# Kernel tuning notes

Hardware: AMD Instinct MI355X
Metric: run time of the kernel (lower is better)

The kernel has to match this reference:

```python
import jax, jax.numpy as jnp
import numpy as np

B, S, D, H = 2, 2048, 1024, 16
HD = D // H  # head_dim = 64
ROPE_BASE = 10000.0


def setup_inputs() -> dict:
    key = jax.random.key(0)
    ks = jax.random.split(key, 5)
    scale = 1.0 / np.sqrt(D)
    return {
        "x": jax.random.normal(ks[0], (B, S, D), dtype=jnp.float32),
        "Wq": jax.random.normal(ks[1], (D, D), dtype=jnp.float32) * scale,
        "Wk": jax.random.normal(ks[2], (D, D), dtype=jnp.float32) * scale,
        "Wv": jax.random.normal(ks[3], (D, D), dtype=jnp.float32) * scale,
        "Wo": jax.random.normal(ks[4], (D, D), dtype=jnp.float32) * scale,
    }


def _rotate_half(x):
    x1, x2 = x[..., : HD // 2], x[..., HD // 2:]
    return jnp.concatenate((-x2, x1), axis=-1)


def _rope_cos_sin(seq_len):
    inv_freq = 1.0 / (ROPE_BASE ** (jnp.arange(0, HD, 2, dtype=jnp.float32) / HD))
    t = jnp.arange(seq_len, dtype=jnp.float32)
    freqs = jnp.outer(t, inv_freq)          # [S, HD/2]
    emb = jnp.concatenate((freqs, freqs), -1)  # [S, HD]
    return jnp.cos(emb), jnp.sin(emb)


def reference(x, Wq, Wk, Wv, Wo):
    # projections (torch Linear: y = x @ W.T), split heads -> [B, H, S, HD]
    def proj(W):
        return (x @ W.T).reshape(B, S, H, HD).transpose(0, 2, 1, 3)

    q, k, v = proj(Wq), proj(Wk), proj(Wv)

    cos, sin = _rope_cos_sin(S)  # [S, HD] each, broadcast over B, H
    q = q * cos + _rotate_half(q) * sin
    k = k * cos + _rotate_half(k) * sin

    scale = 1.0 / np.sqrt(HD)
    scores = jnp.einsum("bhsd,bhtd->bhst", q, k) * scale  # [B,H,S,S]
    attn = jax.nn.softmax(scores, axis=-1)
    out = jnp.einsum("bhst,bhtd->bhsd", attn, v)           # [B,H,S,HD]
    out = out.transpose(0, 2, 1, 3).reshape(B, S, D)
    return out @ Wo.T
```

## Files before the change

kernel.cpp:

```cpp
#include <hip/hip_runtime.h>
#include <hip/hip_bf16.h>
#include <math.h>
#include <stdint.h>

typedef __bf16 bf16;
typedef __bf16 bf16x8 __attribute__((ext_vector_type(8)));
typedef __bf16 bf16x4 __attribute__((ext_vector_type(4)));
typedef float  f32x4  __attribute__((ext_vector_type(4)));

#define MFMA16(a,b,c) __builtin_amdgcn_mfma_f32_16x16x32_bf16((a),(b),(c),0,0,0)
#define GLOAD_LDS16(g, l) \
  __builtin_amdgcn_global_load_lds((__attribute__((address_space(1))) void*)(g), \
                                   (__attribute__((address_space(3))) void*)(l), 16, 0, 0)

static constexpr int kB  = 2;
static constexpr int kS  = 2048;
static constexpr int kD  = 1024;
static constexpr int kH  = 16;
static constexpr int kHD = 64;
static constexpr int kM  = kB * kS;
static constexpr float kExpC = 0.125f * 1.44269504f;

__global__ void cvt_all(const float* __restrict__ x,
                        const float* __restrict__ wq, const float* __restrict__ wk,
                        const float* __restrict__ wv, const float* __restrict__ wo,
                        bf16* __restrict__ xb,
                        bf16* __restrict__ wqb, bf16* __restrict__ wkb,
                        bf16* __restrict__ wvb, bf16* __restrict__ wob,
                        float2* __restrict__ rtab)
{
  const int i = blockIdx.x * 256 + threadIdx.x;
  const int NX4 = (kM * kD) / 4;
  const int NW4 = (kD * kD) / 4;
  if (i >= NX4 + 4 * NW4) {
    const int idx = i - (NX4 + 4 * NW4);
    const int s = idx >> 5, d = idx & 31;
    const float f = exp2f(-(float)d * 0.4152410118609203f);
    float sn, cs;
    sincosf((float)s * f, &sn, &cs);
    rtab[idx] = make_float2(cs, sn);
    return;
  }
  const float* src; bf16* dst; int off;
  if (i < NX4) { src = x; dst = xb; off = i; }
  else {
    const int j = i - NX4;
    const int seg = j >> 18;
    off = j & (NW4 - 1);
    src = (seg == 0) ? wq : (seg == 1) ? wk : (seg == 2) ? wv : wo;
    dst = (seg == 0) ? wqb : (seg == 1) ? wkb : (seg == 2) ? wvb : wob;
  }
  const float4 v = ((const float4*)src)[off];
  bf16x4 o = { (bf16)v.x, (bf16)v.y, (bf16)v.z, (bf16)v.w };
  ((bf16x4*)dst)[off] = o;
}

__device__ __forceinline__ void gemm_core_128(
    const bf16* __restrict__ A, const bf16* __restrict__ Bw,
    int m0, int n0, int K, bf16* aT, bf16* bT, f32x4 acc[4][4])
{
  const int t = threadIdx.x, lane = t & 63, wave = t >> 6;
  const int wm = wave >> 1, wn = wave & 1;
  const int srow = lane >> 2;
  const int scol = (lane & 3) * 8;
  for (int k0 = 0; k0 < K; k0 += 32) {
    __syncthreads();
#pragma unroll
    for (int c = 0; c < 2; ++c) {
      const int row = c * 64 + wave * 16 + srow;
      const bf16* ga = A  + (size_t)(m0 + row) * K + k0 + scol;
      const bf16* gb = Bw + (size_t)(n0 + row) * K + k0 + scol;
      GLOAD_LDS16(ga, aT + c * 2048 + wave * 512);
      GLOAD_LDS16(gb, bT + c * 2048 + wave * 512);
    }
    __syncthreads();
    bf16x8 af[4], bfr[4];
#pragma unroll
    for (int i = 0; i < 4; ++i) {
      af[i]  = *(const bf16x8*)(aT + (wm * 64 + i * 16 + (lane & 15)) * 32 + (lane >> 4) * 8);
      bfr[i] = *(const bf16x8*)(bT + (wn * 64 + i * 16 + (lane & 15)) * 32 + (lane >> 4) * 8);
    }
#pragma unroll
    for (int i = 0; i < 4; ++i)
#pragma unroll
      for (int j = 0; j < 4; ++j)
        acc[i][j] = MFMA16(af[i], bfr[j], acc[i][j]);
  }
}

__global__ __launch_bounds__(256) void proj_qkv(
    const bf16* __restrict__ xb,
    const bf16* __restrict__ wqb, const bf16* __restrict__ wkb, const bf16* __restrict__ wvb,
    bf16* __restrict__ Qb, bf16* __restrict__ Kb, bf16* __restrict__ Vb,
    const float2* __restrict__ rtab)
{
  __shared__ __align__(16) bf16 aT[4096];
  __shared__ __align__(16) bf16 bT[4096];
  const int z = blockIdx.z;
  const bf16* Ww = (z == 0) ? wqb : (z == 1) ? wkb : wvb;
  bf16*       Op = (z == 0) ? Qb  : (z == 1) ? Kb  : Vb;
  const int m0 = blockIdx.x * 128, n0 = blockIdx.y * 128;
  f32x4 acc[4][4] = {};
  gemm_core_128(xb, Ww, m0, n0, kD, aT, bT, acc);

  const int lane = threadIdx.x & 63, wave = threadIdx.x >> 6;
  const int wm = wave >> 1, wn = wave & 1, quad = lane >> 4, lc = lane & 15;
  const int hh = (n0 >> 6) + wn;
  if (z == 2) {
#pragma unroll
    for (int i = 0; i < 4; ++i)
#pragma unroll
      for (int r = 0; r < 4; ++r) {
        const int m = m0 + wm * 64 + i * 16 + quad * 4 + r;
        const int bidx = m >> 11, s = m & 2047;
        bf16* dst = Op + ((size_t)(bidx * kH + hh) * kS + s) * kHD;
#pragma unroll
        for (int j = 0; j < 4; ++j) dst[j * 16 + lc] = (bf16)acc[i][j][r];
      }
  } else {
    const float f = (z == 0) ? kExpC : 1.0f;
#pragma unroll
    for (int j = 0; j < 2; ++j) {
      const int d = j * 16 + lc;
#pragma unroll
      for (int i = 0; i < 4; ++i)
#pragma unroll
        for (int r = 0; r < 4; ++r) {
          const int m = m0 + wm * 64 + i * 16 + quad * 4 + r;
          const int bidx = m >> 11, s = m & 2047;
          const float2 cs = rtab[s * 32 + d];
          const float v0 = acc[i][j][r], v1 = acc[i][j + 2][r];
          bf16* dst = Op + ((size_t)(bidx * kH + hh) * kS + s) * kHD;
          dst[d]      = (bf16)((v0 * cs.x - v1 * cs.y) * f);
          dst[d + 32] = (bf16)((v1 * cs.x + v0 * cs.y) * f);
        }
    }
  }
}

__global__ __launch_bounds__(256) void transpose_v(
    const bf16* __restrict__ Vb, bf16* __restrict__ Vt)
{
  __shared__ __align__(16) bf16 buf[128 * 72];
  const int t = threadIdx.x;
  const int kc = blockIdx.x, bh = blockIdx.y;
  const bf16* src = Vb + ((size_t)bh * kS + kc * 128) * kHD;
  {
    const int srow = t >> 1, half = (t & 1) * 32;
#pragma unroll
    for (int u = 0; u < 4; ++u)
      *(uint4*)&buf[srow * 72 + half + u * 8] = *(const uint4*)(src + srow * kHD + half + u * 8);
  }
  __syncthreads();
  {
    const int d = t & 63, c = t >> 6;
    bf16 tmp[32];
#pragma unroll
    for (int e = 0; e < 32; ++e) tmp[e] = buf[(c * 32 + e) * 72 + d];
    bf16* dst = Vt + ((size_t)bh * kHD + d) * kS + kc * 128 + c * 32;
#pragma unroll
    for (int u = 0; u < 4; ++u)
      *(uint4*)(dst + u * 8) = *(const uint4*)&tmp[u * 8];
  }
}

__global__ __launch_bounds__(256, 2) void attn(
    const bf16* __restrict__ Qb, const bf16* __restrict__ Kb,
    const bf16* __restrict__ Vt, bf16* __restrict__ Ob)
{
  __shared__ __align__(16) bf16 kT[128 * 72];
  __shared__ __align__(16) bf16 vT[64 * 136];
  const int t = threadIdx.x, lane = t & 63, wave = t >> 6;
  const int quad = lane >> 4, lc = lane & 15;
  const int qt = blockIdx.x, bh = blockIdx.y;
  const size_t base = (size_t)bh * kS * kHD;
  const bf16* Qp = Qb + base + (size_t)qt * 128 * kHD;
  const bf16* Kp = Kb + base;
  const bf16* Vp = Vt + base;

  bf16x8 qf[2][2];
#pragma unroll
  for (int tm = 0; tm < 2; ++tm)
#pragma unroll
    for (int ks = 0; ks < 2; ++ks)
      qf[tm][ks] = *(const bf16x8*)(Qp + (wave * 32 + tm * 16 + lc) * kHD + ks * 32 + quad * 8);

  f32x4 oacc[2][4] = {};
  f32x4 lacc[2] = {};
  const bf16 one = (bf16)1.0f;
  const bf16x8 ones = { one, one, one, one, one, one, one, one };

  const int srow = t >> 1, shalf = (t & 1) * 32;
  const int vd = t >> 2, vc = t & 3;

  for (int kt = 0; kt < kS / 128; ++kt) {
    __syncthreads();
    {
      const bf16* ksrc = Kp + (size_t)(kt * 128 + srow) * kHD + shalf;
#pragma unroll
      for (int u = 0; u < 4; ++u)
        *(uint4*)&kT[srow * 72 + shalf + u * 8] = *(const uint4*)(ksrc + u * 8);
      const bf16* vsrc = Vp + (size_t)vd * kS + kt * 128 + vc * 32;
#pragma unroll
      for (int u = 0; u < 4; ++u)
        *(uint4*)&vT[vd * 136 + vc * 32 + u * 8] = *(const uint4*)(vsrc + u * 8);
    }
    __syncthreads();

    bf16x8 kf[8][2];
#pragma unroll
    for (int nk = 0; nk < 8; ++nk)
#pragma unroll
      for (int ks = 0; ks < 2; ++ks)
        kf[nk][ks] = *(const bf16x8*)&kT[(nk * 16 + lc) * 72 + ks * 32 + quad * 8];

    bf16x8 pfrag[2][4];
#pragma unroll
    for (int tm = 0; tm < 2; ++tm) {
      f32x4 sc[8] = {};
#pragma unroll
      for (int nk = 0; nk < 8; ++nk) {
        sc[nk] = MFMA16(kf[nk][0], qf[tm][0], sc[nk]);
        sc[nk] = MFMA16(kf[nk][1], qf[tm][1], sc[nk]);
      }
#pragma unroll
      for (int kp = 0; kp < 4; ++kp) {
        bf16x8 p;
#pragma unroll
        for (int j = 0; j < 4; ++j) {
          p[j]     = (bf16)__builtin_amdgcn_exp2f(sc[2 * kp][j]);
          p[j + 4] = (bf16)__builtin_amdgcn_exp2f(sc[2 * kp + 1][j]);
        }
        pfrag[tm][kp] = p;
      }
    }

#pragma unroll
    for (int kp = 0; kp < 4; ++kp)
#pragma unroll
      for (int tm = 0; tm < 2; ++tm)
        lacc[tm] = MFMA16(pfrag[tm][kp], ones, lacc[tm]);

#pragma unroll
    for (int nd = 0; nd < 4; ++nd)
#pragma unroll
      for (int kp = 0; kp < 4; ++kp) {
        const bf16x4 lo = *(const bf16x4*)&vT[(nd * 16 + lc) * 136 + kp * 32 + quad * 4];
        const bf16x4 hi = *(const bf16x4*)&vT[(nd * 16 + lc) * 136 + kp * 32 + 16 + quad * 4];
        const bf16x8 vfr = __builtin_shufflevector(lo, hi, 0, 1, 2, 3, 4, 5, 6, 7);
#pragma unroll
        for (int tm = 0; tm < 2; ++tm)
          oacc[tm][nd] = MFMA16(pfrag[tm][kp], vfr, oacc[tm][nd]);
      }
  }

  const int b = bh >> 4, h = bh & 15;
#pragma unroll
  for (int tm = 0; tm < 2; ++tm)
#pragma unroll
    for (int r = 0; r < 4; ++r) {
      const float inv = 1.0f / lacc[tm][r];
      const int s = qt * 128 + wave * 32 + tm * 16 + quad * 4 + r;
      bf16* dst = Ob + ((size_t)(b * kS + s)) * kD + h * kHD;
#pragma unroll
      for (int nd = 0; nd < 4; ++nd)
        dst[nd * 16 + lc] = (bf16)(oacc[tm][nd][r] * inv);
    }
}

__global__ __launch_bounds__(256) void out_proj(
    const bf16* __restrict__ Ab, const bf16* __restrict__ wob, float* __restrict__ Cout)
{
  __shared__ __align__(16) bf16 aT[4096];
  __shared__ __align__(16) bf16 bT[4096];
  const int m0 = blockIdx.x * 128, n0 = blockIdx.y * 128;
  f32x4 acc[4][4] = {};
  gemm_core_128(Ab, wob, m0, n0, kD, aT, bT, acc);
  const int lane = threadIdx.x & 63, wave = threadIdx.x >> 6;
  const int wm = wave >> 1, wn = wave & 1, quad = lane >> 4, lc = lane & 15;
#pragma unroll
  for (int i = 0; i < 4; ++i)
#pragma unroll
    for (int r = 0; r < 4; ++r) {
      const int m = m0 + wm * 64 + i * 16 + quad * 4 + r;
#pragma unroll
      for (int j = 0; j < 4; ++j)
        Cout[(size_t)m * kD + n0 + wn * 64 + j * 16 + lc] = acc[i][j][r];
    }
}

extern "C" void kernel_launch(void* const* d_in, const int* in_sizes, int n_in,
                              void* d_out, int out_size, void* d_ws, size_t ws_size,
                              hipStream_t stream)
{
  const float* x  = (const float*)d_in[0];
  const float* wq = (const float*)d_in[1];
  const float* wk = (const float*)d_in[2];
  const float* wv = (const float*)d_in[3];
  const float* wo = (const float*)d_in[4];
  float* out = (float*)d_out;

  char* ws = (char*)d_ws;
  const size_t MB = 1024 * 1024;
  if (ws_size < 57 * MB) return;
  bf16* xb  = (bf16*)(ws + 0 * MB);
  bf16* wqb = (bf16*)(ws + 8 * MB);
  bf16* wkb = (bf16*)(ws + 10 * MB);
  bf16* wvb = (bf16*)(ws + 12 * MB);
  bf16* wob = (bf16*)(ws + 14 * MB);
  bf16* Qb  = (bf16*)(ws + 16 * MB);
  bf16* Kb  = (bf16*)(ws + 24 * MB);
  bf16* Vb  = (bf16*)(ws + 32 * MB);
  bf16* Ob  = (bf16*)(ws + 40 * MB);
  float2* rtab = (float2*)(ws + 48 * MB);
  bf16* Vtp = (bf16*)(ws + 49 * MB);

  cvt_all<<<8448, 256, 0, stream>>>(x, wq, wk, wv, wo, xb, wqb, wkb, wvb, wob, rtab);
  proj_qkv<<<dim3(32, 8, 3), 256, 0, stream>>>(xb, wqb, wkb, wvb, Qb, Kb, Vb, rtab);
  transpose_v<<<dim3(16, 32), 256, 0, stream>>>(Vb, Vtp);
  attn<<<dim3(16, 32), 256, 0, stream>>>(Qb, Kb, Vtp, Ob);
  out_proj<<<dim3(32, 8), 256, 0, stream>>>(Ob, wob, out);
}
```

Baseline: 199.4 us.

## Fuse V transpose into QKV projection epilogue and swizzle attention block order

The V projection epilogue now stages its 128x128 tile in shared memory transposed and writes V directly in [B,H,HD,S] layout. This removes the separate transpose_v kernel launch and its extra global read and write of V. The attention grid is flattened to 1D and blocks are remapped so consecutive blocks work on different heads, which spreads work and K/V cache reuse differently across XCDs. The cost is 34KB of extra LDS in proj_qkv, which may lower its occupancy, plus a block barrier in the V path.

```diff
diff --git a/kernel.cpp b/kernel.cpp
--- a/kernel.cpp
+++ b/kernel.cpp
@@ -91,14 +91,14 @@
 __global__ __launch_bounds__(256) void proj_qkv(
     const bf16* __restrict__ xb,
     const bf16* __restrict__ wqb, const bf16* __restrict__ wkb, const bf16* __restrict__ wvb,
-    bf16* __restrict__ Qb, bf16* __restrict__ Kb, bf16* __restrict__ Vb,
+    bf16* __restrict__ Qb, bf16* __restrict__ Kb, bf16* __restrict__ Vt,
     const float2* __restrict__ rtab)
 {
   __shared__ __align__(16) bf16 aT[4096];
   __shared__ __align__(16) bf16 bT[4096];
+  __shared__ __align__(16) bf16 vtr[2 * 64 * 136];
   const int z = blockIdx.z;
   const bf16* Ww = (z == 0) ? wqb : (z == 1) ? wkb : wvb;
-  bf16*       Op = (z == 0) ? Qb  : (z == 1) ? Kb  : Vb;
   const int m0 = blockIdx.x * 128, n0 = blockIdx.y * 128;
   f32x4 acc[4][4] = {};
   gemm_core_128(xb, Ww, m0, n0, kD, aT, bT, acc);
@@ -110,14 +110,25 @@
 #pragma unroll
     for (int i = 0; i < 4; ++i)
 #pragma unroll
-      for (int r = 0; r < 4; ++r) {
-        const int m = m0 + wm * 64 + i * 16 + quad * 4 + r;
-        const int bidx = m >> 11, s = m & 2047;
-        bf16* dst = Op + ((size_t)(bidx * kH + hh) * kS + s) * kHD;
-#pragma unroll
-        for (int j = 0; j < 4; ++j) dst[j * 16 + lc] = (bf16)acc[i][j][r];
+      for (int j = 0; j < 4; ++j) {
+        bf16x4 p;
+#pragma unroll
+        for (int r = 0; r < 4; ++r) p[r] = (bf16)acc[i][j][r];
+        *(bf16x4*)&vtr[(wn * 64 + j * 16 + lc) * 136 + wm * 64 + i * 16 + quad * 4] = p;
       }
+    __syncthreads();
+    const int t = threadIdx.x;
+    const int row = t >> 1;
+    const int sh = (t & 1) * 64;
+    const int bidx = m0 >> 11;
+    const int hh2 = (n0 >> 6) + (row >> 6);
+    const int d = row & 63;
+    bf16* dst = Vt + ((size_t)(bidx * kH + hh2) * kHD + d) * kS + (m0 & 2047) + sh;
+#pragma unroll
+    for (int u = 0; u < 8; ++u)
+      *(uint4*)(dst + u * 8) = *(const uint4*)&vtr[row * 136 + sh + u * 8];
   } else {
+    bf16* Op = (z == 0) ? Qb : Kb;
     const float f = (z == 0) ? kExpC : 1.0f;
 #pragma unroll
     for (int j = 0; j < 2; ++j) {
@@ -138,32 +149,6 @@
   }
 }
 
-__global__ __launch_bounds__(256) void transpose_v(
-    const bf16* __restrict__ Vb, bf16* __restrict__ Vt)
-{
-  __shared__ __align__(16) bf16 buf[128 * 72];
-  const int t = threadIdx.x;
-  const int kc = blockIdx.x, bh = blockIdx.y;
-  const bf16* src = Vb + ((size_t)bh * kS + kc * 128) * kHD;
-  {
-    const int srow = t >> 1, half = (t & 1) * 32;
-#pragma unroll
-    for (int u = 0; u < 4; ++u)
-      *(uint4*)&buf[srow * 72 + half + u * 8] = *(const uint4*)(src + srow * kHD + half + u * 8);
-  }
-  __syncthreads();
-  {
-    const int d = t & 63, c = t >> 6;
-    bf16 tmp[32];
-#pragma unroll
-    for (int e = 0; e < 32; ++e) tmp[e] = buf[(c * 32 + e) * 72 + d];
-    bf16* dst = Vt + ((size_t)bh * kHD + d) * kS + kc * 128 + c * 32;
-#pragma unroll
-    for (int u = 0; u < 4; ++u)
-      *(uint4*)(dst + u * 8) = *(const uint4*)&tmp[u * 8];
-  }
-}
-
 __global__ __launch_bounds__(256, 2) void attn(
     const bf16* __restrict__ Qb, const bf16* __restrict__ Kb,
     const bf16* __restrict__ Vt, bf16* __restrict__ Ob)
@@ -172,7 +157,9 @@
   __shared__ __align__(16) bf16 vT[64 * 136];
   const int t = threadIdx.x, lane = t & 63, wave = t >> 6;
   const int quad = lane >> 4, lc = lane & 15;
-  const int qt = blockIdx.x, bh = blockIdx.y;
+  const int bid = blockIdx.x;
+  const int qt = (bid >> 3) & 15;
+  const int bh = (bid & 7) * 4 + (bid >> 7);
   const size_t base = (size_t)bh * kS * kHD;
   const bf16* Qp = Qb + base + (size_t)qt * 128 * kHD;
   const bf16* Kp = Kb + base;
@@ -310,14 +297,12 @@
   bf16* wob = (bf16*)(ws + 14 * MB);
   bf16* Qb  = (bf16*)(ws + 16 * MB);
   bf16* Kb  = (bf16*)(ws + 24 * MB);
-  bf16* Vb  = (bf16*)(ws + 32 * MB);
   bf16* Ob  = (bf16*)(ws + 40 * MB);
   float2* rtab = (float2*)(ws + 48 * MB);
   bf16* Vtp = (bf16*)(ws + 49 * MB);
 
   cvt_all<<<8448, 256, 0, stream>>>(x, wq, wk, wv, wo, xb, wqb, wkb, wvb, wob, rtab);
-  proj_qkv<<<dim3(32, 8, 3), 256, 0, stream>>>(xb, wqb, wkb, wvb, Qb, Kb, Vb, rtab);
-  transpose_v<<<dim3(16, 32), 256, 0, stream>>>(Vb, Vtp);
-  attn<<<dim3(16, 32), 256, 0, stream>>>(Qb, Kb, Vtp, Ob);
+  proj_qkv<<<dim3(32, 8, 3), 256, 0, stream>>>(xb, wqb, wkb, wvb, Qb, Kb, Vtp, rtab);
+  attn<<<dim3(512), 256, 0, stream>>>(Qb, Kb, Vtp, Ob);
   out_proj<<<dim3(32, 8), 256, 0, stream>>>(Ob, wob, out);
 }
```

After: 194.0 us. 1.03x faster.
